# Optimization experiments

Hardware: AMD Instinct MI355X
Metric: run time of the kernel (lower is better)

Reference implementation:

```python
import jax, jax.numpy as jnp
import numpy as np

N = 50000      # nodes
E = 800000     # edges
DIN = 128      # in_channels
H = 128        # hidden_channels
G = 64         # graphs in batch
OUT = 8        # head out_channels


def setup_inputs() -> dict:
    key = jax.random.key(0)
    ks = jax.random.split(key, 12)
    s = 0.1  # weight init scale
    x = jax.random.normal(ks[0], (N, DIN), jnp.float32)
    edge_index = jax.random.randint(ks[1], (2, E), 0, N, dtype=jnp.int64)
    batch = jnp.sort(jax.random.randint(ks[2], (N,), 0, G, dtype=jnp.int64))
    W0 = jax.random.normal(ks[3], (DIN, H), jnp.float32) * s
    b0 = jnp.zeros((H,), jnp.float32)
    W1 = jax.random.normal(ks[4], (H, H), jnp.float32) * s
    b1 = jnp.zeros((H,), jnp.float32)
    W2 = jax.random.normal(ks[5], (H, H), jnp.float32) * s
    b2 = jnp.zeros((H,), jnp.float32)
    Wh = jax.random.normal(ks[6], (H, OUT), jnp.float32) * s
    bh = jnp.zeros((OUT,), jnp.float32)
    return {"x": x, "edge_index": edge_index, "batch": batch,
            "W0": W0, "b0": b0, "W1": W1, "b1": b1, "W2": W2, "b2": b2,
            "Wh": Wh, "bh": bh}


def gcn_conv(x, src, dst, W, b):
    # GCNConv with self-loops and symmetric normalization (PyG defaults).
    h = x @ W                                           # [N, H]
    deg = jnp.zeros((N,), h.dtype).at[dst].add(1.0) + 1.0   # in-degree incl. self-loop
    dinv = jax.lax.rsqrt(deg)                           # deg^{-1/2}
    coef = dinv[src] * dinv[dst]                        # [E]
    agg = jnp.zeros_like(h).at[dst].add(h[src] * coef[:, None])
    # self-loop contribution: dinv[i]^2 * h[i]
    return agg + h * (dinv * dinv)[:, None] + b


def reference(x, edge_index, batch, W0, b0, W1, b1, W2, b2, Wh, bh):
    src, dst = edge_index[0], edge_index[1]
    h = jax.nn.relu(gcn_conv(x, src, dst, W0, b0))
    h = jax.nn.relu(gcn_conv(h, src, dst, W1, b1))
    h = gcn_conv(h, src, dst, W2, b2)                   # last layer: no activation
    # global mean pool over graphs
    sums = jnp.zeros((G, H), h.dtype).at[batch].add(h)
    cnt = jnp.zeros((G,), h.dtype).at[batch].add(1.0)
    pooled = sums / jnp.maximum(cnt, 1.0)[:, None]      # [G, H]
    return pooled @ Wh + bh                             # [G, OUT]
```

## Files before the change

kernel.cpp:

```cpp
#include <hip/hip_runtime.h>

#define N_NODES 50000
#define N_EDGES 800000
#define HD 128
#define NGRAPH 64
#define NOUT 8
#define SLOTS 64
#define GAGRID 3125
#define EPB 2048

typedef __attribute__((ext_vector_type(8))) short bf8_t;
typedef __attribute__((ext_vector_type(4))) float f4_t;
typedef __attribute__((ext_vector_type(8))) unsigned short us8;

__device__ __forceinline__ unsigned short f2b(float f) {
    unsigned u = __float_as_uint(f);
    u += 0x7fffu + ((u >> 16) & 1u);
    return (unsigned short)(u >> 16);
}
__device__ __forceinline__ float b2f(unsigned short h) {
    return __uint_as_float(((unsigned)h) << 16);
}

__global__ __launch_bounds__(256) void cvtw_k(const float* __restrict__ W0,
                                              const float* __restrict__ W1,
                                              const float* __restrict__ W2,
                                              unsigned short* __restrict__ WT,
                                              int* __restrict__ degc,
                                              float* __restrict__ sums,
                                              float* __restrict__ cnt) {
    int idx = blockIdx.x * 256 + threadIdx.x;
    if (idx < 3 * HD * HD) {
        int w = idx >> 14;
        int rem = idx & 16383;
        int n = rem >> 7;
        int k = rem & 127;
        const float* W = (w == 0) ? W0 : (w == 1) ? W1 : W2;
        WT[(size_t)w * HD * HD + n * HD + k] = f2b(W[k * HD + n]);
    }
    if (idx < N_NODES) degc[idx] = 0;
    if (idx < NGRAPH * HD) sums[idx] = 0.f;
    if (idx < NGRAPH) cnt[idx] = 0.f;
}

__global__ __launch_bounds__(256) void fillx_k(const int* __restrict__ src,
                                               const int* __restrict__ dst,
                                               int* __restrict__ degc,
                                               unsigned short* __restrict__ slots) {
    const int p = blockIdx.x & 7;
    const int c = blockIdx.x >> 3;
    const int e0 = c * EPB;
    int e1 = e0 + EPB; if (e1 > N_EDGES) e1 = N_EDGES;
    for (int e = e0 + threadIdx.x; e < e1; e += 256) {
        int d = dst[e];
        if (((d >> 4) & 7) == p) {
            int s = src[e];
            int pos = atomicAdd(&degc[d], 1);
            if (pos < SLOTS)
                slots[(size_t)d * SLOTS + pos] = (unsigned short)s;
        }
    }
}

__global__ __launch_bounds__(256) void mm_f32in_k(const float* __restrict__ X,
                                                  const unsigned short* __restrict__ WT,
                                                  const int* __restrict__ degc,
                                                  unsigned short* __restrict__ Y) {
    const int lane = threadIdx.x & 63;
    const int wave = threadIdx.x >> 6;
    const int r = lane & 15;
    const int q = lane >> 4;
    const int row0 = blockIdx.x * 64 + wave * 16;
    int arow = row0 + r; if (arow >= N_NODES) arow = N_NODES - 1;

    f4_t acc[8];
#pragma unroll
    for (int n = 0; n < 8; ++n) acc[n] = (f4_t){0.f, 0.f, 0.f, 0.f};

#pragma unroll
    for (int kb = 0; kb < 4; ++kb) {
        f4_t fa = __builtin_nontemporal_load((const f4_t*)(X + (size_t)arow * HD + kb * 32 + q * 8));
        f4_t fb = __builtin_nontemporal_load((const f4_t*)(X + (size_t)arow * HD + kb * 32 + q * 8 + 4));
        bf8_t a;
        a[0] = (short)f2b(fa[0]); a[1] = (short)f2b(fa[1]);
        a[2] = (short)f2b(fa[2]); a[3] = (short)f2b(fa[3]);
        a[4] = (short)f2b(fb[0]); a[5] = (short)f2b(fb[1]);
        a[6] = (short)f2b(fb[2]); a[7] = (short)f2b(fb[3]);
#pragma unroll
        for (int n = 0; n < 8; ++n) {
            bf8_t b = *(const bf8_t*)(WT + (size_t)(n * 16 + r) * HD + kb * 32 + q * 8);
            acc[n] = __builtin_amdgcn_mfma_f32_16x16x32_bf16(a, b, acc[n], 0, 0, 0);
        }
    }
    const int orow = row0 + q * 4;
#pragma unroll
    for (int i = 0; i < 4; ++i) {
        int rr = orow + i;
        if (rr < N_NODES) {
            float dv = rsqrtf((float)degc[rr] + 1.0f);
#pragma unroll
            for (int n = 0; n < 8; ++n)
                Y[(size_t)rr * HD + n * 16 + r] = f2b(acc[n][i] * dv);
        }
    }
}

__global__ __launch_bounds__(256) void fusedGM2_k(const unsigned short* __restrict__ T,
                                                  const int* __restrict__ degc,
                                                  const unsigned short* __restrict__ slots,
                                                  const float* __restrict__ bias,
                                                  const unsigned short* __restrict__ WT,
                                                  unsigned short* __restrict__ Y) {
    __shared__ unsigned short hs[16][136];
    const int tid = threadIdx.x;
    const int base = blockIdx.x * 16;

    {
        const int g = tid >> 4;
        const int l = tid & 15;
        const int j8 = l * 8;
        const int i = base + g;
        const int dg = degc[i];
        int dc = dg; if (dc > SLOTS) dc = SLOTS;
        const float di = rsqrtf((float)dg + 1.0f);
        const unsigned short* sl = slots + (size_t)i * SLOTS;

        float a[8];
#pragma unroll
        for (int k = 0; k < 8; ++k) a[k] = 0.f;
        int e = 0;
        for (; e + 15 < dc; e += 16) {
            us8 i0 = *(const us8*)(sl + e);
            us8 i1 = *(const us8*)(sl + e + 8);
            us8 v[16];
#pragma unroll
            for (int u = 0; u < 8; ++u) v[u]     = *(const us8*)(T + (size_t)i0[u] * HD + j8);
#pragma unroll
            for (int u = 0; u < 8; ++u) v[u + 8] = *(const us8*)(T + (size_t)i1[u] * HD + j8);
#pragma unroll
            for (int u = 0; u < 16; ++u) {
#pragma unroll
                for (int k = 0; k < 8; ++k) a[k] += b2f(v[u][k]);
            }
        }
        if (e < dc) {
            us8 i0 = *(const us8*)(sl + e);
            us8 i1 = *(const us8*)(sl + e + 8);
            const unsigned short safe = i0[0];
            int s[16]; float m[16];
#pragma unroll
            for (int u = 0; u < 8; ++u) {
                m[u] = (e + u < dc) ? 1.f : 0.f;
                s[u] = (e + u < dc) ? i0[u] : safe;
            }
#pragma unroll
            for (int u = 0; u < 8; ++u) {
                m[u + 8] = (e + 8 + u < dc) ? 1.f : 0.f;
                s[u + 8] = (e + 8 + u < dc) ? i1[u] : safe;
            }
            us8 v[16];
#pragma unroll
            for (int u = 0; u < 16; ++u) v[u] = *(const us8*)(T + (size_t)s[u] * HD + j8);
#pragma unroll
            for (int u = 0; u < 16; ++u) {
#pragma unroll
                for (int k = 0; k < 8; ++k) a[k] = fmaf(m[u], b2f(v[u][k]), a[k]);
            }
        }
        us8 tv = *(const us8*)(T + (size_t)i * HD + j8);
        float4 bv0 = *(const float4*)(bias + j8);
        float4 bv1 = *(const float4*)(bias + j8 + 4);
        float bb[8] = {bv0.x, bv0.y, bv0.z, bv0.w, bv1.x, bv1.y, bv1.z, bv1.w};
        us8 o;
#pragma unroll
        for (int k = 0; k < 8; ++k) {
            float r = di * (a[k] + b2f(tv[k])) + bb[k];
            r = fmaxf(r, 0.f);
            o[k] = f2b(r);
        }
        *(us8*)(&hs[g][j8]) = o;
    }
    __syncthreads();

    {
        const int lane = tid & 63;
        const int wave = tid >> 6;
        const int r = lane & 15;
        const int q = lane >> 4;
        const int n0 = wave * 2;

        f4_t acc0 = (f4_t){0.f, 0.f, 0.f, 0.f};
        f4_t acc1 = (f4_t){0.f, 0.f, 0.f, 0.f};
#pragma unroll
        for (int kb = 0; kb < 4; ++kb) {
            bf8_t a = *(const bf8_t*)(&hs[r][kb * 32 + q * 8]);
            bf8_t b0 = *(const bf8_t*)(WT + (size_t)(n0 * 16 + r) * HD + kb * 32 + q * 8);
            bf8_t b1 = *(const bf8_t*)(WT + (size_t)(n0 * 16 + 16 + r) * HD + kb * 32 + q * 8);
            acc0 = __builtin_amdgcn_mfma_f32_16x16x32_bf16(a, b0, acc0, 0, 0, 0);
            acc1 = __builtin_amdgcn_mfma_f32_16x16x32_bf16(a, b1, acc1, 0, 0, 0);
        }
#pragma unroll
        for (int i = 0; i < 4; ++i) {
            int rr = base + q * 4 + i;
            float dv = rsqrtf((float)degc[rr] + 1.0f);
            Y[(size_t)rr * HD + n0 * 16 + r]      = f2b(acc0[i] * dv);
            Y[(size_t)rr * HD + n0 * 16 + 16 + r] = f2b(acc1[i] * dv);
        }
    }
}

__global__ __launch_bounds__(256) void gather_k(const unsigned short* __restrict__ T,
                                                const int* __restrict__ degc,
                                                const unsigned short* __restrict__ slots,
                                                const float* __restrict__ b,
                                                unsigned short* __restrict__ out) {
    int i = blockIdx.x * 16 + (threadIdx.x >> 4);
    if (i >= N_NODES) return;
    const int j8 = (threadIdx.x & 15) * 8;
    const int dg = degc[i];
    int dc = dg; if (dc > SLOTS) dc = SLOTS;
    const float di = rsqrtf((float)dg + 1.0f);
    const unsigned short* sl = slots + (size_t)i * SLOTS;

    float a[8];
#pragma unroll
    for (int k = 0; k < 8; ++k) a[k] = 0.f;
    int e = 0;
    for (; e + 15 < dc; e += 16) {
        us8 i0 = *(const us8*)(sl + e);
        us8 i1 = *(const us8*)(sl + e + 8);
        us8 v[16];
#pragma unroll
        for (int u = 0; u < 8; ++u) v[u]     = *(const us8*)(T + (size_t)i0[u] * HD + j8);
#pragma unroll
        for (int u = 0; u < 8; ++u) v[u + 8] = *(const us8*)(T + (size_t)i1[u] * HD + j8);
#pragma unroll
        for (int u = 0; u < 16; ++u) {
#pragma unroll
            for (int k = 0; k < 8; ++k) a[k] += b2f(v[u][k]);
        }
    }
    if (e < dc) {
        us8 i0 = *(const us8*)(sl + e);
        us8 i1 = *(const us8*)(sl + e + 8);
        const unsigned short safe = i0[0];
        int s[16]; float m[16];
#pragma unroll
        for (int u = 0; u < 8; ++u) {
            m[u] = (e + u < dc) ? 1.f : 0.f;
            s[u] = (e + u < dc) ? i0[u] : safe;
        }
#pragma unroll
        for (int u = 0; u < 8; ++u) {
            m[u + 8] = (e + 8 + u < dc) ? 1.f : 0.f;
            s[u + 8] = (e + 8 + u < dc) ? i1[u] : safe;
        }
        us8 v[16];
#pragma unroll
        for (int u = 0; u < 16; ++u) v[u] = *(const us8*)(T + (size_t)s[u] * HD + j8);
#pragma unroll
        for (int u = 0; u < 16; ++u) {
#pragma unroll
            for (int k = 0; k < 8; ++k) a[k] = fmaf(m[u], b2f(v[u][k]), a[k]);
        }
    }
    us8 tv = *(const us8*)(T + (size_t)i * HD + j8);
    float4 bv0 = *(const float4*)(b + j8);
    float4 bv1 = *(const float4*)(b + j8 + 4);
    float bb[8] = {bv0.x, bv0.y, bv0.z, bv0.w, bv1.x, bv1.y, bv1.z, bv1.w};
    us8 o;
#pragma unroll
    for (int k = 0; k < 8; ++k)
        o[k] = f2b(di * (a[k] + b2f(tv[k])) + bb[k]);
    *(us8*)(out + (size_t)i * HD + j8) = o;
}

__global__ __launch_bounds__(256) void pool2_k(const unsigned short* __restrict__ H2,
                                               const int* __restrict__ batch,
                                               float* __restrict__ sums,
                                               float* __restrict__ cnt) {
    const int t = threadIdx.x;
    const int f = t & 127;
    const int half = t >> 7;
    int i0 = blockIdx.x * 128 + half * 64;
    if (i0 >= N_NODES) return;
    int i1 = i0 + 64; if (i1 > N_NODES) i1 = N_NODES;

    int cur = batch[i0];
    float acc = 0.f;
    float c = 0.f;
    for (int i = i0; i < i1; ++i) {
        int g = batch[i];
        if (g != cur) {
            atomicAdd(&sums[cur * HD + f], acc);
            if (f == 0) atomicAdd(&cnt[cur], c);
            acc = 0.f; c = 0.f; cur = g;
        }
        acc += b2f(H2[(size_t)i * HD + f]);
        c += 1.f;
    }
    atomicAdd(&sums[cur * HD + f], acc);
    if (f == 0) atomicAdd(&cnt[cur], c);
}

__global__ __launch_bounds__(512) void head_k(const float* __restrict__ sums,
                                              const float* __restrict__ cnt,
                                              const float* __restrict__ Wh,
                                              const float* __restrict__ bh,
                                              float* __restrict__ out) {
    int t = threadIdx.x;
    int g = t >> 3, o = t & 7;
    float inv = 1.0f / fmaxf(cnt[g], 1.0f);
    float acc = bh[o];
    for (int h = 0; h < HD; ++h)
        acc += sums[g * HD + h] * inv * Wh[h * NOUT + o];
    out[g * NOUT + o] = acc;
}

extern "C" void kernel_launch(void* const* d_in, const int* in_sizes, int n_in,
                              void* d_out, int out_size, void* d_ws, size_t ws_size,
                              hipStream_t stream) {
    const float* x  = (const float*)d_in[0];
    const int*   ei = (const int*)d_in[1];
    const int*   batch = (const int*)d_in[2];
    const float* W0 = (const float*)d_in[3];
    const float* b0 = (const float*)d_in[4];
    const float* W1 = (const float*)d_in[5];
    const float* b1 = (const float*)d_in[6];
    const float* W2 = (const float*)d_in[7];
    const float* b2 = (const float*)d_in[8];
    const float* Wh = (const float*)d_in[9];
    const float* bh = (const float*)d_in[10];
    float* out = (float*)d_out;

    const int* src = ei;
    const int* dst = ei + N_EDGES;

    char* wsb = (char*)d_ws;
    int*            degc  = (int*)(wsb + 0);
    unsigned short* slots = (unsigned short*)(wsb + 200000);
    unsigned short* WT    = (unsigned short*)(wsb + 6600000);
    unsigned short* A     = (unsigned short*)(wsb + 6698304);
    unsigned short* C     = (unsigned short*)(wsb + 19498304);
    float*          sums  = (float*)(wsb + 32298304);
    float*          cnt   = (float*)(wsb + 32331072);

    const int mmGrid = (N_NODES + 63) / 64;
    const int fillxGrid = ((N_EDGES + EPB - 1) / EPB) * 8;

    cvtw_k<<<(N_NODES + 255) / 256, 256, 0, stream>>>(W0, W1, W2, WT, degc, sums, cnt);

    fillx_k<<<fillxGrid, 256, 0, stream>>>(src, dst, degc, slots);

    mm_f32in_k<<<mmGrid, 256, 0, stream>>>(x, WT, degc, A);

    fusedGM2_k<<<GAGRID, 256, 0, stream>>>(A, degc, slots, b0, WT + HD * HD, C);

    fusedGM2_k<<<GAGRID, 256, 0, stream>>>(C, degc, slots, b1, WT + 2 * HD * HD, A);

    gather_k<<<GAGRID, 256, 0, stream>>>(A, degc, slots, b2, C);

    pool2_k<<<(N_NODES + 127) / 128, 256, 0, stream>>>(C, batch, sums, cnt);
    head_k<<<1, 512, 0, stream>>>(sums, cnt, Wh, bh, out);
}
```

Before: 299.0 us.

## Split fused gather+GEMM into column-sliced gather and separate bf16 GEMM kernels

Replaces the fused gather-then-MFMA kernel with two kernels: a gather kernel where each block handles one 32-column slice for 64 nodes, and a standalone bf16 MFMA GEMM. Column slicing is meant to make the random row gathers from T fit better in cache, because concurrently running blocks touch only a quarter of each row. It also uses nontemporal loads for the slot indices and degrees. In exchange it adds two extra launches and writes and re-reads the intermediate activations through global memory, and each node's index list is now read once per slice.

```diff
diff --git a/kernel.cpp b/kernel.cpp
--- a/kernel.cpp
+++ b/kernel.cpp
@@ -6,7 +6,6 @@
 #define NGRAPH 64
 #define NOUT 8
 #define SLOTS 64
-#define GAGRID 3125
 #define EPB 2048
 
 typedef __attribute__((ext_vector_type(8))) short bf8_t;
@@ -105,119 +104,60 @@
     }
 }
 
-__global__ __launch_bounds__(256) void fusedGM2_k(const unsigned short* __restrict__ T,
-                                                  const int* __restrict__ degc,
-                                                  const unsigned short* __restrict__ slots,
-                                                  const float* __restrict__ bias,
-                                                  const unsigned short* __restrict__ WT,
-                                                  unsigned short* __restrict__ Y) {
-    __shared__ unsigned short hs[16][136];
-    const int tid = threadIdx.x;
-    const int base = blockIdx.x * 16;
-
-    {
-        const int g = tid >> 4;
-        const int l = tid & 15;
-        const int j8 = l * 8;
-        const int i = base + g;
-        const int dg = degc[i];
-        int dc = dg; if (dc > SLOTS) dc = SLOTS;
-        const float di = rsqrtf((float)dg + 1.0f);
-        const unsigned short* sl = slots + (size_t)i * SLOTS;
-
-        float a[8];
-#pragma unroll
-        for (int k = 0; k < 8; ++k) a[k] = 0.f;
-        int e = 0;
-        for (; e + 15 < dc; e += 16) {
-            us8 i0 = *(const us8*)(sl + e);
-            us8 i1 = *(const us8*)(sl + e + 8);
-            us8 v[16];
-#pragma unroll
-            for (int u = 0; u < 8; ++u) v[u]     = *(const us8*)(T + (size_t)i0[u] * HD + j8);
-#pragma unroll
-            for (int u = 0; u < 8; ++u) v[u + 8] = *(const us8*)(T + (size_t)i1[u] * HD + j8);
-#pragma unroll
-            for (int u = 0; u < 16; ++u) {
-#pragma unroll
-                for (int k = 0; k < 8; ++k) a[k] += b2f(v[u][k]);
-            }
-        }
-        if (e < dc) {
-            us8 i0 = *(const us8*)(sl + e);
-            us8 i1 = *(const us8*)(sl + e + 8);
-            const unsigned short safe = i0[0];
-            int s[16]; float m[16];
-#pragma unroll
-            for (int u = 0; u < 8; ++u) {
-                m[u] = (e + u < dc) ? 1.f : 0.f;
-                s[u] = (e + u < dc) ? i0[u] : safe;
-            }
-#pragma unroll
-            for (int u = 0; u < 8; ++u) {
-                m[u + 8] = (e + 8 + u < dc) ? 1.f : 0.f;
-                s[u + 8] = (e + 8 + u < dc) ? i1[u] : safe;
-            }
-            us8 v[16];
-#pragma unroll
-            for (int u = 0; u < 16; ++u) v[u] = *(const us8*)(T + (size_t)s[u] * HD + j8);
-#pragma unroll
-            for (int u = 0; u < 16; ++u) {
-#pragma unroll
-                for (int k = 0; k < 8; ++k) a[k] = fmaf(m[u], b2f(v[u][k]), a[k]);
-            }
-        }
-        us8 tv = *(const us8*)(T + (size_t)i * HD + j8);
-        float4 bv0 = *(const float4*)(bias + j8);
-        float4 bv1 = *(const float4*)(bias + j8 + 4);
-        float bb[8] = {bv0.x, bv0.y, bv0.z, bv0.w, bv1.x, bv1.y, bv1.z, bv1.w};
-        us8 o;
-#pragma unroll
-        for (int k = 0; k < 8; ++k) {
-            float r = di * (a[k] + b2f(tv[k])) + bb[k];
-            r = fmaxf(r, 0.f);
-            o[k] = f2b(r);
-        }
-        *(us8*)(&hs[g][j8]) = o;
-    }
-    __syncthreads();
-
-    {
-        const int lane = tid & 63;
-        const int wave = tid >> 6;
-        const int r = lane & 15;
-        const int q = lane >> 4;
-        const int n0 = wave * 2;
-
-        f4_t acc0 = (f4_t){0.f, 0.f, 0.f, 0.f};
-        f4_t acc1 = (f4_t){0.f, 0.f, 0.f, 0.f};
-#pragma unroll
-        for (int kb = 0; kb < 4; ++kb) {
-            bf8_t a = *(const bf8_t*)(&hs[r][kb * 32 + q * 8]);
-            bf8_t b0 = *(const bf8_t*)(WT + (size_t)(n0 * 16 + r) * HD + kb * 32 + q * 8);
-            bf8_t b1 = *(const bf8_t*)(WT + (size_t)(n0 * 16 + 16 + r) * HD + kb * 32 + q * 8);
-            acc0 = __builtin_amdgcn_mfma_f32_16x16x32_bf16(a, b0, acc0, 0, 0, 0);
-            acc1 = __builtin_amdgcn_mfma_f32_16x16x32_bf16(a, b1, acc1, 0, 0, 0);
-        }
-#pragma unroll
-        for (int i = 0; i < 4; ++i) {
-            int rr = base + q * 4 + i;
+__global__ __launch_bounds__(256) void mm_bf_k(const unsigned short* __restrict__ S,
+                                               const unsigned short* __restrict__ WT,
+                                               const int* __restrict__ degc,
+                                               unsigned short* __restrict__ Y) {
+    const int lane = threadIdx.x & 63;
+    const int wave = threadIdx.x >> 6;
+    const int r = lane & 15;
+    const int q = lane >> 4;
+    const int row0 = blockIdx.x * 64 + wave * 16;
+    int arow = row0 + r; if (arow >= N_NODES) arow = N_NODES - 1;
+
+    f4_t acc[8];
+#pragma unroll
+    for (int n = 0; n < 8; ++n) acc[n] = (f4_t){0.f, 0.f, 0.f, 0.f};
+
+#pragma unroll
+    for (int kb = 0; kb < 4; ++kb) {
+        bf8_t a = *(const bf8_t*)(S + (size_t)arow * HD + kb * 32 + q * 8);
+#pragma unroll
+        for (int n = 0; n < 8; ++n) {
+            bf8_t b = *(const bf8_t*)(WT + (size_t)(n * 16 + r) * HD + kb * 32 + q * 8);
+            acc[n] = __builtin_amdgcn_mfma_f32_16x16x32_bf16(a, b, acc[n], 0, 0, 0);
+        }
+    }
+    const int orow = row0 + q * 4;
+#pragma unroll
+    for (int i = 0; i < 4; ++i) {
+        int rr = orow + i;
+        if (rr < N_NODES) {
             float dv = rsqrtf((float)degc[rr] + 1.0f);
-            Y[(size_t)rr * HD + n0 * 16 + r]      = f2b(acc0[i] * dv);
-            Y[(size_t)rr * HD + n0 * 16 + 16 + r] = f2b(acc1[i] * dv);
-        }
-    }
-}
-
-__global__ __launch_bounds__(256) void gather_k(const unsigned short* __restrict__ T,
+#pragma unroll
+            for (int n = 0; n < 8; ++n)
+                Y[(size_t)rr * HD + n * 16 + r] = f2b(acc[n][i] * dv);
+        }
+    }
+}
+
+__global__ __launch_bounds__(256) void gslice_k(const unsigned short* __restrict__ T,
                                                 const int* __restrict__ degc,
                                                 const unsigned short* __restrict__ slots,
-                                                const float* __restrict__ b,
-                                                unsigned short* __restrict__ out) {
-    int i = blockIdx.x * 16 + (threadIdx.x >> 4);
+                                                const float* __restrict__ bias,
+                                                unsigned short* __restrict__ S,
+                                                int relu) {
+    const int p = blockIdx.x & 7;
+    const int chunk = blockIdx.x >> 3;
+    const int slice = p & 3;
+    const int half = p >> 2;
+    const int g = threadIdx.x >> 2;
+    const int l = threadIdx.x & 3;
+    const int i = chunk * 128 + half * 64 + g;
     if (i >= N_NODES) return;
-    const int j8 = (threadIdx.x & 15) * 8;
-    const int dg = degc[i];
+    const int col = slice * 32 + l * 8;
+
+    const int dg = __builtin_nontemporal_load(degc + i);
     int dc = dg; if (dc > SLOTS) dc = SLOTS;
     const float di = rsqrtf((float)dg + 1.0f);
     const unsigned short* sl = slots + (size_t)i * SLOTS;
@@ -227,13 +167,13 @@
     for (int k = 0; k < 8; ++k) a[k] = 0.f;
     int e = 0;
     for (; e + 15 < dc; e += 16) {
-        us8 i0 = *(const us8*)(sl + e);
-        us8 i1 = *(const us8*)(sl + e + 8);
+        us8 i0 = __builtin_nontemporal_load((const us8*)(sl + e));
+        us8 i1 = __builtin_nontemporal_load((const us8*)(sl + e + 8));
         us8 v[16];
 #pragma unroll
-        for (int u = 0; u < 8; ++u) v[u]     = *(const us8*)(T + (size_t)i0[u] * HD + j8);
-#pragma unroll
-        for (int u = 0; u < 8; ++u) v[u + 8] = *(const us8*)(T + (size_t)i1[u] * HD + j8);
+        for (int u = 0; u < 8; ++u) v[u]     = *(const us8*)(T + (size_t)i0[u] * HD + col);
+#pragma unroll
+        for (int u = 0; u < 8; ++u) v[u + 8] = *(const us8*)(T + (size_t)i1[u] * HD + col);
 #pragma unroll
         for (int u = 0; u < 16; ++u) {
 #pragma unroll
@@ -241,8 +181,8 @@
         }
     }
     if (e < dc) {
-        us8 i0 = *(const us8*)(sl + e);
-        us8 i1 = *(const us8*)(sl + e + 8);
+        us8 i0 = __builtin_nontemporal_load((const us8*)(sl + e));
+        us8 i1 = __builtin_nontemporal_load((const us8*)(sl + e + 8));
         const unsigned short safe = i0[0];
         int s[16]; float m[16];
 #pragma unroll
@@ -257,22 +197,25 @@
         }
         us8 v[16];
 #pragma unroll
-        for (int u = 0; u < 16; ++u) v[u] = *(const us8*)(T + (size_t)s[u] * HD + j8);
+        for (int u = 0; u < 16; ++u) v[u] = *(const us8*)(T + (size_t)s[u] * HD + col);
 #pragma unroll
         for (int u = 0; u < 16; ++u) {
 #pragma unroll
             for (int k = 0; k < 8; ++k) a[k] = fmaf(m[u], b2f(v[u][k]), a[k]);
         }
     }
-    us8 tv = *(const us8*)(T + (size_t)i * HD + j8);
-    float4 bv0 = *(const float4*)(b + j8);
-    float4 bv1 = *(const float4*)(b + j8 + 4);
+    us8 tv = *(const us8*)(T + (size_t)i * HD + col);
+    float4 bv0 = *(const float4*)(bias + col);
+    float4 bv1 = *(const float4*)(bias + col + 4);
     float bb[8] = {bv0.x, bv0.y, bv0.z, bv0.w, bv1.x, bv1.y, bv1.z, bv1.w};
     us8 o;
 #pragma unroll
-    for (int k = 0; k < 8; ++k)
-        o[k] = f2b(di * (a[k] + b2f(tv[k])) + bb[k]);
-    *(us8*)(out + (size_t)i * HD + j8) = o;
+    for (int k = 0; k < 8; ++k) {
+        float r = di * (a[k] + b2f(tv[k])) + bb[k];
+        if (relu) r = fmaxf(r, 0.f);
+        o[k] = f2b(r);
+    }
+    *(us8*)(S + (size_t)i * HD + col) = o;
 }
 
 __global__ __launch_bounds__(256) void pool2_k(const unsigned short* __restrict__ H2,
@@ -345,8 +288,9 @@
     float*          sums  = (float*)(wsb + 32298304);
     float*          cnt   = (float*)(wsb + 32331072);
 
-    const int mmGrid = (N_NODES + 63) / 64;
+    const int mmGrid   = (N_NODES + 63) / 64;
     const int fillxGrid = ((N_EDGES + EPB - 1) / EPB) * 8;
+    const int gslGrid  = ((N_NODES + 127) / 128) * 8;
 
     cvtw_k<<<(N_NODES + 255) / 256, 256, 0, stream>>>(W0, W1, W2, WT, degc, sums, cnt);
 
@@ -354,11 +298,13 @@
 
     mm_f32in_k<<<mmGrid, 256, 0, stream>>>(x, WT, degc, A);
 
-    fusedGM2_k<<<GAGRID, 256, 0, stream>>>(A, degc, slots, b0, WT + HD * HD, C);
-
-    fusedGM2_k<<<GAGRID, 256, 0, stream>>>(C, degc, slots, b1, WT + 2 * HD * HD, A);
-
-    gather_k<<<GAGRID, 256, 0, stream>>>(A, degc, slots, b2, C);
+    gslice_k<<<gslGrid, 256, 0, stream>>>(A, degc, slots, b0, C, 1);
+    mm_bf_k<<<mmGrid, 256, 0, stream>>>(C, WT + HD * HD, degc, A);
+
+    gslice_k<<<gslGrid, 256, 0, stream>>>(A, degc, slots, b1, C, 1);
+    mm_bf_k<<<mmGrid, 256, 0, stream>>>(C, WT + 2 * HD * HD, degc, A);
+
+    gslice_k<<<gslGrid, 256, 0, stream>>>(A, degc, slots, b2, C, 0);
 
     pool2_k<<<(N_NODES + 127) / 128, 256, 0, stream>>>(C, batch, sums, cnt);
     head_k<<<1, 512, 0, stream>>>(sums, cnt, Wh, bh, out);
```

Result: slower. 357.6 us (+19.6%).
